# Kernel tuning notes

Measured on AMD Instinct MI355X. Metric: run time of the kernel, lower is better.

Reference implementation:

```python
import jax, jax.numpy as jnp
import numpy as np

NUM_HEADS = 16
THETA = 10000.0


def _rope(x, pos):
    # x: [..., S, D_h], pos: [S] (broadcastable over leading dims)
    dh = x.shape[-1]
    inv_freq = THETA ** (-jnp.arange(0, dh, 2, dtype=x.dtype) / dh)  # [dh/2]
    ang = pos.astype(x.dtype)[..., None] * inv_freq                   # [S, dh/2]
    cos, sin = jnp.cos(ang), jnp.sin(ang)
    x1, x2 = x[..., ::2], x[..., 1::2]
    out = jnp.stack([x1 * cos - x2 * sin, x1 * sin + x2 * cos], axis=-1)
    return out.reshape(x.shape)


def setup_inputs() -> dict:
    key = jax.random.key(0)
    ks = jax.random.split(key, 5)
    B, S, D = 4, 2048, 1024
    return {
        "in_features": jax.random.normal(ks[0], (B, S, D), dtype=jnp.float32),
        "token_positions": jnp.arange(S, dtype=jnp.int32),
        "wq": jax.random.normal(ks[1], (D, D), dtype=jnp.float32) * 0.02,
        "wk": jax.random.normal(ks[2], (D, D), dtype=jnp.float32) * 0.02,
        "wv": jax.random.normal(ks[3], (D, D), dtype=jnp.float32) * 0.02,
        "wo": jax.random.normal(ks[4], (D, D), dtype=jnp.float32) * 0.02,
    }


def reference(in_features, token_positions, wq, wk, wv, wo):
    B, S, D = in_features.shape
    H = NUM_HEADS
    dh = D // H

    def split_heads(y):  # [B,S,D] -> [B,H,S,dh]  ('s (h d) -> h s d')
        return y.reshape(B, S, H, dh).transpose(0, 2, 1, 3)

    Q = split_heads(in_features @ wq.T)
    K = split_heads(in_features @ wk.T)
    V = split_heads(in_features @ wv.T)

    Q = _rope(Q, token_positions)
    K = _rope(K, token_positions)

    scale = 1.0 / jnp.sqrt(jnp.asarray(dh, dtype=Q.dtype))
    scores = jnp.einsum("bhqd,bhkd->bhqk", Q, K) * scale  # [B,H,S,S]
    causal = jnp.tril(jnp.ones((S, S), dtype=bool))
    scores = jnp.where(causal, scores, -jnp.inf)
    attn = jax.nn.softmax(scores, axis=-1)
    out = jnp.einsum("bhqk,bhkd->bhqd", attn, V)          # [B,H,S,dh]
    out = out.transpose(0, 2, 1, 3).reshape(B, S, D)      # 'h s d -> s (h d)'
    return out @ wo.T
```

## Files before the change

### kernel.cpp

```cpp
#include <hip/hip_runtime.h>
#include <hip/hip_bf16.h>
#include <cmath>

#define BB 4
#define SS 2048
#define DD 1024
#define HH 16
#define DH 64
#define LDK 72

typedef __attribute__((ext_vector_type(8))) short short8;
typedef __attribute__((ext_vector_type(4))) float floatx4;
typedef unsigned short u16;
typedef unsigned int u32;

#define QSCALE 0.18033688011112042f

__device__ __forceinline__ u16 f2bf(float f) {
    union { float f; u32 i; } u; u.f = f;
    u32 r = u.i + 0x7fff + ((u.i >> 16) & 1);
    return (u16)(r >> 16);
}

__device__ __forceinline__ u32 pack_bf16(float a, float b) {
    union { float f; u32 i; } ua, ub; ua.f = a; ub.f = b;
    return __builtin_amdgcn_perm(ub.i + 0x8000u, ua.i + 0x8000u, 0x07060302u);
}

#if !__has_builtin(__builtin_amdgcn_exp2f)
#define __builtin_amdgcn_exp2f exp2f
#endif

__global__ __launch_bounds__(256)
void cast_x(const float* __restrict__ s, u16* __restrict__ d)
{
    int i = (blockIdx.x * 256 + threadIdx.x) * 8;
    float4 f0 = *(const float4*)(s + i);
    float4 f1 = *(const float4*)(s + i + 4);
    u32 o[4];
    o[0] = pack_bf16(f0.x, f0.y); o[1] = pack_bf16(f0.z, f0.w);
    o[2] = pack_bf16(f1.x, f1.y); o[3] = pack_bf16(f1.z, f1.w);
    *(short8*)(d + i) = *(short8*)o;
}

__global__ __launch_bounds__(256)
void cast_w(const float* __restrict__ w0, const float* __restrict__ w1,
            const float* __restrict__ w2, const float* __restrict__ w3,
            u16* __restrict__ o0, u16* __restrict__ o1,
            u16* __restrict__ o2, u16* __restrict__ o3)
{
    const float* s = (blockIdx.y == 0) ? w0 : (blockIdx.y == 1) ? w1 : (blockIdx.y == 2) ? w2 : w3;
    u16* d        = (blockIdx.y == 0) ? o0 : (blockIdx.y == 1) ? o1 : (blockIdx.y == 2) ? o2 : o3;
    int i = (blockIdx.x * 256 + threadIdx.x) * 8;
    float4 f0 = *(const float4*)(s + i);
    float4 f1 = *(const float4*)(s + i + 4);
    u32 o[4];
    o[0] = pack_bf16(f0.x, f0.y); o[1] = pack_bf16(f0.z, f0.w);
    o[2] = pack_bf16(f1.x, f1.y); o[3] = pack_bf16(f1.z, f1.w);
    *(short8*)(d + i) = *(short8*)o;
}

__global__ __launch_bounds__(256)
void gemm_qkv(const u16* __restrict__ Xb,
              const u16* __restrict__ Wq, const u16* __restrict__ Wk, const u16* __restrict__ Wv,
              const int* __restrict__ pos,
              u16* __restrict__ Qb, u16* __restrict__ Kb, u16* __restrict__ Vtb)
{
    __shared__ __align__(16) u16 As[128 * LDK];
    __shared__ __align__(16) u16 Bs[128 * LDK];

    const int tid  = threadIdx.x;
    const int lane = tid & 63, w = tid >> 6;
    const int quad = lane >> 4, l16 = lane & 15;
    const int wr = w >> 1, wc = w & 1;
    const int m0 = blockIdx.x * 128, n0 = blockIdx.y * 128;
    const int which = blockIdx.z;
    const u16* __restrict__ W = (which == 0) ? Wq : (which == 1) ? Wk : Wv;

    const int srow = tid >> 3;
    const int skc  = (tid & 7) << 3;

    floatx4 acc[4][4];
    #pragma unroll
    for (int i = 0; i < 4; i++)
        #pragma unroll
        for (int j = 0; j < 4; j++) acc[i][j] = (floatx4)0.f;

    short8 pa[4], pb[4];
    #pragma unroll
    for (int i = 0; i < 4; i++) {
        int row = srow + i * 32;
        pa[i] = *(const short8*)(Xb + (size_t)(m0 + row) * DD + skc);
        pb[i] = *(const short8*)(W  + (size_t)(n0 + row) * DD + skc);
    }

    for (int kb = 0; kb < DD; kb += 64) {
        __syncthreads();
        #pragma unroll
        for (int i = 0; i < 4; i++) {
            int row = srow + i * 32;
            *(short8*)&As[row * LDK + skc] = pa[i];
            *(short8*)&Bs[row * LDK + skc] = pb[i];
        }
        __syncthreads();
        if (kb + 64 < DD) {
            #pragma unroll
            for (int i = 0; i < 4; i++) {
                int row = srow + i * 32;
                pa[i] = *(const short8*)(Xb + (size_t)(m0 + row) * DD + kb + 64 + skc);
                pb[i] = *(const short8*)(W  + (size_t)(n0 + row) * DD + kb + 64 + skc);
            }
        }
        #pragma unroll
        for (int ks = 0; ks < 2; ks++) {
            short8 a[4], b[4];
            #pragma unroll
            for (int mi = 0; mi < 4; mi++)
                a[mi] = *(const short8*)&As[(wr * 64 + mi * 16 + l16) * LDK + ks * 32 + quad * 8];
            #pragma unroll
            for (int ni = 0; ni < 4; ni++)
                b[ni] = *(const short8*)&Bs[(wc * 64 + ni * 16 + l16) * LDK + ks * 32 + quad * 8];
            #pragma unroll
            for (int mi = 0; mi < 4; mi++)
                #pragma unroll
                for (int ni = 0; ni < 4; ni++)
                    acc[mi][ni] = __builtin_amdgcn_mfma_f32_16x16x32_bf16(a[mi], b[ni], acc[mi][ni], 0, 0, 0);
        }
    }

    const int colbase = n0 + wc * 64 + l16;
    const int rowbase = m0 + wr * 64 + quad * 4;
    u16* __restrict__ OutQK = (which == 0) ? Qb : Kb;

    #pragma unroll
    for (int ni = 0; ni < 4; ni++) {
        int col = colbase + ni * 16;
        int h = col >> 6, d = col & 63;
        float fr = __powf(10000.0f, -(float)(d & ~1) / 64.0f);
        bool evn = (d & 1) == 0;
        #pragma unroll
        for (int mi = 0; mi < 4; mi++) {
            int row0 = rowbase + mi * 16;
            if (which == 2) {
                int b = row0 >> 11, s0 = row0 & (SS - 1);
                ushort4 uv;
                uv.x = f2bf(acc[mi][ni][0]);
                uv.y = f2bf(acc[mi][ni][1]);
                uv.z = f2bf(acc[mi][ni][2]);
                uv.w = f2bf(acc[mi][ni][3]);
                *(ushort4*)&Vtb[((size_t)((b * HH + h) * DH + d)) * SS + s0] = uv;
            } else {
                #pragma unroll
                for (int r = 0; r < 4; r++) {
                    int row = row0 + r;
                    int b = row >> 11, s = row & (SS - 1);
                    float v = acc[mi][ni][r];
                    float other = __shfl_xor(v, 1);
                    float ang = (float)pos[s] * fr;
                    float sn, cs;
                    __sincosf(ang, &sn, &cs);
                    float res = evn ? (v * cs - other * sn) : (other * sn + v * cs);
                    if (which == 0) res *= QSCALE;
                    OutQK[((size_t)((b * HH + h) * SS + s)) * DH + d] = f2bf(res);
                }
            }
        }
    }
}

__global__ __launch_bounds__(256)
void flash_mfma(const u16* __restrict__ Qb, const u16* __restrict__ Kb,
                const u16* __restrict__ Vtb, u16* __restrict__ AOb)
{
    __shared__ __align__(16) u16 Ks[64 * LDK];
    __shared__ __align__(16) u16 Vs[64 * LDK];
    __shared__ __align__(16) u16 Ps[4][16 * LDK];

    const int tid  = threadIdx.x;
    const int lane = tid & 63, w = tid >> 6;
    const int quad = lane >> 4, l16 = lane & 15;
    const int qt = blockIdx.x, bh = blockIdx.y;
    const int b = bh >> 4, h = bh & 15;
    const size_t baseQK = (size_t)bh * SS * DH;
    const size_t baseVt = (size_t)bh * DH * SS;

    const int srow = tid >> 3;
    const int skc  = (tid & 7) << 3;

    const u16* Qp = Qb + baseQK + (size_t)(qt * 64 + w * 16 + l16) * DH;
    short8 qf[2];
    qf[0] = *(const short8*)(Qp + quad * 8);
    qf[1] = *(const short8*)(Qp + 32 + quad * 8);

    float m_run = -__builtin_inff(), l_run = 0.f;
    floatx4 oacc[4];
    #pragma unroll
    for (int ni = 0; ni < 4; ni++) oacc[ni] = (floatx4)0.f;

    const int qloc = w * 16 + l16;

    short8 kr[2], vr[2];
    #pragma unroll
    for (int i = 0; i < 2; i++) {
        int row = srow + i * 32;
        kr[i] = *(const short8*)(Kb + baseQK + (size_t)row * DH + skc);
        vr[i] = *(const short8*)(Vtb + baseVt + (size_t)row * SS + skc);
    }

    for (int kt = 0; kt <= qt; kt++) {
        __syncthreads();
        #pragma unroll
        for (int i = 0; i < 2; i++) {
            int row = srow + i * 32;
            *(short8*)&Ks[row * LDK + skc] = kr[i];
            *(short8*)&Vs[row * LDK + skc] = vr[i];
        }
        __syncthreads();
        if (kt < qt) {
            #pragma unroll
            for (int i = 0; i < 2; i++) {
                int row = srow + i * 32;
                kr[i] = *(const short8*)(Kb + baseQK + (size_t)((kt + 1) * 64 + row) * DH + skc);
                vr[i] = *(const short8*)(Vtb + baseVt + (size_t)row * SS + (kt + 1) * 64 + skc);
            }
        }

        floatx4 sacc[4];
        #pragma unroll
        for (int ni = 0; ni < 4; ni++) sacc[ni] = (floatx4)0.f;
        #pragma unroll
        for (int ks = 0; ks < 2; ks++) {
            #pragma unroll
            for (int ni = 0; ni < 4; ni++) {
                short8 kf = *(const short8*)&Ks[(ni * 16 + l16) * LDK + ks * 32 + quad * 8];
                sacc[ni] = __builtin_amdgcn_mfma_f32_16x16x32_bf16(kf, qf[ks], sacc[ni], 0, 0, 0);
            }
        }

        if (kt == qt) {
            #pragma unroll
            for (int ni = 0; ni < 4; ni++)
                #pragma unroll
                for (int r = 0; r < 4; r++)
                    if (ni * 16 + quad * 4 + r > qloc) sacc[ni][r] = -__builtin_inff();
        }

        float mx01 = fmaxf(fmaxf(sacc[0][0], sacc[0][1]), fmaxf(sacc[0][2], sacc[0][3]));
        float mx23 = fmaxf(fmaxf(sacc[1][0], sacc[1][1]), fmaxf(sacc[1][2], sacc[1][3]));
        float mx45 = fmaxf(fmaxf(sacc[2][0], sacc[2][1]), fmaxf(sacc[2][2], sacc[2][3]));
        float mx67 = fmaxf(fmaxf(sacc[3][0], sacc[3][1]), fmaxf(sacc[3][2], sacc[3][3]));
        float mx = fmaxf(fmaxf(mx01, mx23), fmaxf(mx45, mx67));
        mx = fmaxf(mx, __shfl_xor(mx, 16));
        mx = fmaxf(mx, __shfl_xor(mx, 32));
        float mnew = fmaxf(m_run, mx);
        float al = __builtin_amdgcn_exp2f(m_run - mnew);

        float rs = 0.f;
        #pragma unroll
        for (int ni = 0; ni < 4; ni++) {
            float p0 = __builtin_amdgcn_exp2f(sacc[ni][0] - mnew);
            float p1 = __builtin_amdgcn_exp2f(sacc[ni][1] - mnew);
            float p2 = __builtin_amdgcn_exp2f(sacc[ni][2] - mnew);
            float p3 = __builtin_amdgcn_exp2f(sacc[ni][3] - mnew);
            rs += (p0 + p1) + (p2 + p3);
            u32 pk[2];
            pk[0] = pack_bf16(p0, p1);
            pk[1] = pack_bf16(p2, p3);
            *(uint2*)&Ps[w][l16 * LDK + ni * 16 + quad * 4] = *(uint2*)pk;
        }
        l_run = l_run * al + rs;
        m_run = mnew;

        #pragma unroll
        for (int ni = 0; ni < 4; ni++) oacc[ni] *= al;
        #pragma unroll
        for (int ks = 0; ks < 2; ks++) {
            short8 pb = *(const short8*)&Ps[w][l16 * LDK + ks * 32 + quad * 8];
            #pragma unroll
            for (int ni = 0; ni < 4; ni++) {
                short8 vf = *(const short8*)&Vs[(ni * 16 + l16) * LDK + ks * 32 + quad * 8];
                oacc[ni] = __builtin_amdgcn_mfma_f32_16x16x32_bf16(vf, pb, oacc[ni], 0, 0, 0);
            }
        }
    }

    float l_tot = l_run;
    l_tot += __shfl_xor(l_tot, 16);
    l_tot += __shfl_xor(l_tot, 32);
    const float invl = 1.f / l_tot;
    const int srow_o = qt * 64 + w * 16 + l16;
    u16* dst = AOb + (size_t)(b * SS + srow_o) * DD + h * DH;
    #pragma unroll
    for (int ni = 0; ni < 4; ni++) {
        u32 uo[2];
        uo[0] = pack_bf16(oacc[ni][0] * invl, oacc[ni][1] * invl);
        uo[1] = pack_bf16(oacc[ni][2] * invl, oacc[ni][3] * invl);
        *(uint2*)(dst + ni * 16 + quad * 4) = *(uint2*)uo;
    }
}

__global__ __launch_bounds__(256)
void gemm_out(const u16* __restrict__ A, const u16* __restrict__ W, float* __restrict__ C)
{
    __shared__ __align__(16) u16 As[128 * LDK];
    __shared__ __align__(16) u16 Bs[128 * LDK];

    const int tid  = threadIdx.x;
    const int lane = tid & 63, w = tid >> 6;
    const int quad = lane >> 4, l16 = lane & 15;
    const int wr = w >> 1, wc = w & 1;
    const int m0 = blockIdx.x * 128, n0 = blockIdx.y * 128;

    const int srow = tid >> 3;
    const int skc  = (tid & 7) << 3;

    floatx4 acc[4][4];
    #pragma unroll
    for (int i = 0; i < 4; i++)
        #pragma unroll
        for (int j = 0; j < 4; j++) acc[i][j] = (floatx4)0.f;

    short8 pa[4], pb[4];
    #pragma unroll
    for (int i = 0; i < 4; i++) {
        int row = srow + i * 32;
        pa[i] = *(const short8*)(A + (size_t)(m0 + row) * DD + skc);
        pb[i] = *(const short8*)(W + (size_t)(n0 + row) * DD + skc);
    }

    for (int kb = 0; kb < DD; kb += 64) {
        __syncthreads();
        #pragma unroll
        for (int i = 0; i < 4; i++) {
            int row = srow + i * 32;
            *(short8*)&As[row * LDK + skc] = pa[i];
            *(short8*)&Bs[row * LDK + skc] = pb[i];
        }
        __syncthreads();
        if (kb + 64 < DD) {
            #pragma unroll
            for (int i = 0; i < 4; i++) {
                int row = srow + i * 32;
                pa[i] = *(const short8*)(A + (size_t)(m0 + row) * DD + kb + 64 + skc);
                pb[i] = *(const short8*)(W + (size_t)(n0 + row) * DD + kb + 64 + skc);
            }
        }
        #pragma unroll
        for (int ks = 0; ks < 2; ks++) {
            short8 a[4], b[4];
            #pragma unroll
            for (int mi = 0; mi < 4; mi++)
                a[mi] = *(const short8*)&As[(wr * 64 + mi * 16 + l16) * LDK + ks * 32 + quad * 8];
            #pragma unroll
            for (int ni = 0; ni < 4; ni++)
                b[ni] = *(const short8*)&Bs[(wc * 64 + ni * 16 + l16) * LDK + ks * 32 + quad * 8];
            #pragma unroll
            for (int mi = 0; mi < 4; mi++)
                #pragma unroll
                for (int ni = 0; ni < 4; ni++)
                    acc[mi][ni] = __builtin_amdgcn_mfma_f32_16x16x32_bf16(a[mi], b[ni], acc[mi][ni], 0, 0, 0);
        }
    }

    const int colbase = n0 + wc * 64 + l16;
    const int rowbase = m0 + wr * 64 + quad * 4;
    #pragma unroll
    for (int ni = 0; ni < 4; ni++) {
        int col = colbase + ni * 16;
        #pragma unroll
        for (int mi = 0; mi < 4; mi++) {
            int row0 = rowbase + mi * 16;
            #pragma unroll
            for (int r = 0; r < 4; r++)
                C[(size_t)(row0 + r) * DD + col] = acc[mi][ni][r];
        }
    }
}

extern "C" void kernel_launch(void* const* d_in, const int* in_sizes, int n_in,
                              void* d_out, int out_size, void* d_ws, size_t ws_size,
                              hipStream_t stream) {
    const float* X  = (const float*)d_in[0];
    const int* pos  = (const int*)d_in[1];
    const float* wq = (const float*)d_in[2];
    const float* wk = (const float*)d_in[3];
    const float* wv = (const float*)d_in[4];
    const float* wo = (const float*)d_in[5];
    float* out = (float*)d_out;

    const size_t wsz = (size_t)DD * DD;
    const size_t qsz = (size_t)BB * HH * SS * DH;
    u16* Wqb = (u16*)d_ws;
    u16* Wkb = Wqb + wsz;
    u16* Wvb = Wkb + wsz;
    u16* Wob = Wvb + wsz;
    u16* Qb  = Wob + wsz;
    u16* Kb  = Qb + qsz;
    u16* Vtb = Kb + qsz;
    u16* Xb  = Vtb + qsz;
    u16* AOb = Xb;

    dim3 blk(256);
    cast_x<<<dim3(BB * SS * DD / 2048), blk, 0, stream>>>(X, Xb);
    cast_w<<<dim3(DD * DD / 2048, 4), blk, 0, stream>>>(wq, wk, wv, wo, Wqb, Wkb, Wvb, Wob);
    gemm_qkv<<<dim3((BB * SS) / 128, DD / 128, 3), blk, 0, stream>>>(Xb, Wqb, Wkb, Wvb, pos, Qb, Kb, Vtb);
    flash_mfma<<<dim3(SS / 64, BB * HH), blk, 0, stream>>>(Qb, Kb, Vtb, AOb);
    gemm_out<<<dim3((BB * SS) / 128, DD / 128), blk, 0, stream>>>(AOb, Wob, out);
}
```

Measured before the change: 329.8 us.

## Pair mirrored causal query tiles per block to balance flash attention work

Each flash-attention block now handles two query tiles, qt and its mirror (31-qt), so every block does the same amount of causal work. The two tiles share the staged K/V tiles in shared memory, and the grid is halved to 16x64 blocks. This removes the tail imbalance of causal attention and cuts K/V reloads for the lower tile. In exchange it doubles the accumulator registers, which may lower occupancy, and it leaves only 1024 blocks on the device.

```diff
diff --git a/kernel.cpp b/kernel.cpp
--- a/kernel.cpp
+++ b/kernel.cpp
@@ -168,18 +168,84 @@
     }
 }
 
+__device__ __forceinline__ void attn_step(
+    const u16* Ks, const u16* Vs, u16* Psw,
+    const short8* qf, floatx4* oacc, float& m_run, float& l_run,
+    const int l16, const int quad, const bool diag, const int qloc)
+{
+    floatx4 sacc[4];
+    #pragma unroll
+    for (int ni = 0; ni < 4; ni++) sacc[ni] = (floatx4)0.f;
+    #pragma unroll
+    for (int ks = 0; ks < 2; ks++) {
+        #pragma unroll
+        for (int ni = 0; ni < 4; ni++) {
+            short8 kf = *(const short8*)&Ks[(ni * 16 + l16) * LDK + ks * 32 + quad * 8];
+            sacc[ni] = __builtin_amdgcn_mfma_f32_16x16x32_bf16(kf, qf[ks], sacc[ni], 0, 0, 0);
+        }
+    }
+
+    if (diag) {
+        #pragma unroll
+        for (int ni = 0; ni < 4; ni++)
+            #pragma unroll
+            for (int r = 0; r < 4; r++)
+                if (ni * 16 + quad * 4 + r > qloc) sacc[ni][r] = -__builtin_inff();
+    }
+
+    float mx01 = fmaxf(fmaxf(sacc[0][0], sacc[0][1]), fmaxf(sacc[0][2], sacc[0][3]));
+    float mx23 = fmaxf(fmaxf(sacc[1][0], sacc[1][1]), fmaxf(sacc[1][2], sacc[1][3]));
+    float mx45 = fmaxf(fmaxf(sacc[2][0], sacc[2][1]), fmaxf(sacc[2][2], sacc[2][3]));
+    float mx67 = fmaxf(fmaxf(sacc[3][0], sacc[3][1]), fmaxf(sacc[3][2], sacc[3][3]));
+    float mx = fmaxf(fmaxf(mx01, mx23), fmaxf(mx45, mx67));
+    mx = fmaxf(mx, __shfl_xor(mx, 16));
+    mx = fmaxf(mx, __shfl_xor(mx, 32));
+    float mnew = fmaxf(m_run, mx);
+    float al = __builtin_amdgcn_exp2f(m_run - mnew);
+
+    float rs = 0.f;
+    #pragma unroll
+    for (int ni = 0; ni < 4; ni++) {
+        float p0 = __builtin_amdgcn_exp2f(sacc[ni][0] - mnew);
+        float p1 = __builtin_amdgcn_exp2f(sacc[ni][1] - mnew);
+        float p2 = __builtin_amdgcn_exp2f(sacc[ni][2] - mnew);
+        float p3 = __builtin_amdgcn_exp2f(sacc[ni][3] - mnew);
+        rs += (p0 + p1) + (p2 + p3);
+        u32 pk[2];
+        pk[0] = pack_bf16(p0, p1);
+        pk[1] = pack_bf16(p2, p3);
+        *(uint2*)&Psw[l16 * LDK + ni * 16 + quad * 4] = *(uint2*)pk;
+    }
+    l_run = l_run * al + rs;
+    m_run = mnew;
+
+    #pragma unroll
+    for (int ni = 0; ni < 4; ni++) oacc[ni] *= al;
+    #pragma unroll
+    for (int ks = 0; ks < 2; ks++) {
+        short8 pb = *(const short8*)&Psw[l16 * LDK + ks * 32 + quad * 8];
+        #pragma unroll
+        for (int ni = 0; ni < 4; ni++) {
+            short8 vf = *(const short8*)&Vs[(ni * 16 + l16) * LDK + ks * 32 + quad * 8];
+            oacc[ni] = __builtin_amdgcn_mfma_f32_16x16x32_bf16(vf, pb, oacc[ni], 0, 0, 0);
+        }
+    }
+}
+
 __global__ __launch_bounds__(256)
 void flash_mfma(const u16* __restrict__ Qb, const u16* __restrict__ Kb,
                 const u16* __restrict__ Vtb, u16* __restrict__ AOb)
 {
     __shared__ __align__(16) u16 Ks[64 * LDK];
     __shared__ __align__(16) u16 Vs[64 * LDK];
-    __shared__ __align__(16) u16 Ps[4][16 * LDK];
+    __shared__ __align__(16) u16 Ps[4][2][16 * LDK];
 
     const int tid  = threadIdx.x;
     const int lane = tid & 63, w = tid >> 6;
     const int quad = lane >> 4, l16 = lane & 15;
-    const int qt = blockIdx.x, bh = blockIdx.y;
+    const int qtA = blockIdx.x;
+    const int qtB = (SS / 64 - 1) - blockIdx.x;
+    const int bh = blockIdx.y;
     const int b = bh >> 4, h = bh & 15;
     const size_t baseQK = (size_t)bh * SS * DH;
     const size_t baseVt = (size_t)bh * DH * SS;
@@ -187,15 +253,19 @@
     const int srow = tid >> 3;
     const int skc  = (tid & 7) << 3;
 
-    const u16* Qp = Qb + baseQK + (size_t)(qt * 64 + w * 16 + l16) * DH;
-    short8 qf[2];
-    qf[0] = *(const short8*)(Qp + quad * 8);
-    qf[1] = *(const short8*)(Qp + 32 + quad * 8);
-
-    float m_run = -__builtin_inff(), l_run = 0.f;
-    floatx4 oacc[4];
-    #pragma unroll
-    for (int ni = 0; ni < 4; ni++) oacc[ni] = (floatx4)0.f;
+    const u16* QpA = Qb + baseQK + (size_t)(qtA * 64 + w * 16 + l16) * DH;
+    const u16* QpB = Qb + baseQK + (size_t)(qtB * 64 + w * 16 + l16) * DH;
+    short8 qfA[2], qfB[2];
+    qfA[0] = *(const short8*)(QpA + quad * 8);
+    qfA[1] = *(const short8*)(QpA + 32 + quad * 8);
+    qfB[0] = *(const short8*)(QpB + quad * 8);
+    qfB[1] = *(const short8*)(QpB + 32 + quad * 8);
+
+    float mA = -__builtin_inff(), lA = 0.f;
+    float mB = -__builtin_inff(), lB = 0.f;
+    floatx4 oaccA[4], oaccB[4];
+    #pragma unroll
+    for (int ni = 0; ni < 4; ni++) { oaccA[ni] = (floatx4)0.f; oaccB[ni] = (floatx4)0.f; }
 
     const int qloc = w * 16 + l16;
 
@@ -207,7 +277,7 @@
         vr[i] = *(const short8*)(Vtb + baseVt + (size_t)row * SS + skc);
     }
 
-    for (int kt = 0; kt <= qt; kt++) {
+    for (int kt = 0; kt <= qtB; kt++) {
         __syncthreads();
         #pragma unroll
         for (int i = 0; i < 2; i++) {
@@ -216,7 +286,7 @@
             *(short8*)&Vs[row * LDK + skc] = vr[i];
         }
         __syncthreads();
-        if (kt < qt) {
+        if (kt < qtB) {
             #pragma unroll
             for (int i = 0; i < 2; i++) {
                 int row = srow + i * 32;
@@ -225,77 +295,33 @@
             }
         }
 
-        floatx4 sacc[4];
-        #pragma unroll
-        for (int ni = 0; ni < 4; ni++) sacc[ni] = (floatx4)0.f;
-        #pragma unroll
-        for (int ks = 0; ks < 2; ks++) {
-            #pragma unroll
-            for (int ni = 0; ni < 4; ni++) {
-                short8 kf = *(const short8*)&Ks[(ni * 16 + l16) * LDK + ks * 32 + quad * 8];
-                sacc[ni] = __builtin_amdgcn_mfma_f32_16x16x32_bf16(kf, qf[ks], sacc[ni], 0, 0, 0);
-            }
-        }
-
-        if (kt == qt) {
-            #pragma unroll
-            for (int ni = 0; ni < 4; ni++)
-                #pragma unroll
-                for (int r = 0; r < 4; r++)
-                    if (ni * 16 + quad * 4 + r > qloc) sacc[ni][r] = -__builtin_inff();
-        }
-
-        float mx01 = fmaxf(fmaxf(sacc[0][0], sacc[0][1]), fmaxf(sacc[0][2], sacc[0][3]));
-        float mx23 = fmaxf(fmaxf(sacc[1][0], sacc[1][1]), fmaxf(sacc[1][2], sacc[1][3]));
-        float mx45 = fmaxf(fmaxf(sacc[2][0], sacc[2][1]), fmaxf(sacc[2][2], sacc[2][3]));
-        float mx67 = fmaxf(fmaxf(sacc[3][0], sacc[3][1]), fmaxf(sacc[3][2], sacc[3][3]));
-        float mx = fmaxf(fmaxf(mx01, mx23), fmaxf(mx45, mx67));
-        mx = fmaxf(mx, __shfl_xor(mx, 16));
-        mx = fmaxf(mx, __shfl_xor(mx, 32));
-        float mnew = fmaxf(m_run, mx);
-        float al = __builtin_amdgcn_exp2f(m_run - mnew);
-
-        float rs = 0.f;
-        #pragma unroll
-        for (int ni = 0; ni < 4; ni++) {
-            float p0 = __builtin_amdgcn_exp2f(sacc[ni][0] - mnew);
-            float p1 = __builtin_amdgcn_exp2f(sacc[ni][1] - mnew);
-            float p2 = __builtin_amdgcn_exp2f(sacc[ni][2] - mnew);
-            float p3 = __builtin_amdgcn_exp2f(sacc[ni][3] - mnew);
-            rs += (p0 + p1) + (p2 + p3);
-            u32 pk[2];
-            pk[0] = pack_bf16(p0, p1);
-            pk[1] = pack_bf16(p2, p3);
-            *(uint2*)&Ps[w][l16 * LDK + ni * 16 + quad * 4] = *(uint2*)pk;
-        }
-        l_run = l_run * al + rs;
-        m_run = mnew;
-
-        #pragma unroll
-        for (int ni = 0; ni < 4; ni++) oacc[ni] *= al;
-        #pragma unroll
-        for (int ks = 0; ks < 2; ks++) {
-            short8 pb = *(const short8*)&Ps[w][l16 * LDK + ks * 32 + quad * 8];
-            #pragma unroll
-            for (int ni = 0; ni < 4; ni++) {
-                short8 vf = *(const short8*)&Vs[(ni * 16 + l16) * LDK + ks * 32 + quad * 8];
-                oacc[ni] = __builtin_amdgcn_mfma_f32_16x16x32_bf16(vf, pb, oacc[ni], 0, 0, 0);
-            }
-        }
-    }
-
-    float l_tot = l_run;
-    l_tot += __shfl_xor(l_tot, 16);
-    l_tot += __shfl_xor(l_tot, 32);
-    const float invl = 1.f / l_tot;
-    const int srow_o = qt * 64 + w * 16 + l16;
-    u16* dst = AOb + (size_t)(b * SS + srow_o) * DD + h * DH;
+        if (kt <= qtA)
+            attn_step(Ks, Vs, &Ps[w][0][0], qfA, oaccA, mA, lA,
+                      l16, quad, kt == qtA, qloc);
+        attn_step(Ks, Vs, &Ps[w][1][0], qfB, oaccB, mB, lB,
+                  l16, quad, kt == qtB, qloc);
+    }
+
+    float lAt = lA;
+    lAt += __shfl_xor(lAt, 16);
+    lAt += __shfl_xor(lAt, 32);
+    float lBt = lB;
+    lBt += __shfl_xor(lBt, 16);
+    lBt += __shfl_xor(lBt, 32);
+    const float invlA = 1.f / lAt;
+    const float invlB = 1.f / lBt;
+
+    u16* dstA = AOb + (size_t)(b * SS + qtA * 64 + w * 16 + l16) * DD + h * DH;
+    u16* dstB = AOb + (size_t)(b * SS + qtB * 64 + w * 16 + l16) * DD + h * DH;
     #pragma unroll
     for (int ni = 0; ni < 4; ni++) {
         u32 uo[2];
-        uo[0] = pack_bf16(oacc[ni][0] * invl, oacc[ni][1] * invl);
-        uo[1] = pack_bf16(oacc[ni][2] * invl, oacc[ni][3] * invl);
-        *(uint2*)(dst + ni * 16 + quad * 4) = *(uint2*)uo;
+        uo[0] = pack_bf16(oaccA[ni][0] * invlA, oaccA[ni][1] * invlA);
+        uo[1] = pack_bf16(oaccA[ni][2] * invlA, oaccA[ni][3] * invlA);
+        *(uint2*)(dstA + ni * 16 + quad * 4) = *(uint2*)uo;
+        uo[0] = pack_bf16(oaccB[ni][0] * invlB, oaccB[ni][1] * invlB);
+        uo[1] = pack_bf16(oaccB[ni][2] * invlB, oaccB[ni][3] * invlB);
+        *(uint2*)(dstB + ni * 16 + quad * 4) = *(uint2*)uo;
     }
 }
 
@@ -404,6 +430,6 @@
     cast_x<<<dim3(BB * SS * DD / 2048), blk, 0, stream>>>(X, Xb);
     cast_w<<<dim3(DD * DD / 2048, 4), blk, 0, stream>>>(wq, wk, wv, wo, Wqb, Wkb, Wvb, Wob);
     gemm_qkv<<<dim3((BB * SS) / 128, DD / 128, 3), blk, 0, stream>>>(Xb, Wqb, Wkb, Wvb, pos, Qb, Kb, Vtb);
-    flash_mfma<<<dim3(SS / 64, BB * HH), blk, 0, stream>>>(Qb, Kb, Vtb, AOb);
+    flash_mfma<<<dim3(SS / 128, BB * HH), blk, 0, stream>>>(Qb, Kb, Vtb, AOb);
     gemm_out<<<dim3((BB * SS) / 128, DD / 128), blk, 0, stream>>>(AOb, Wob, out);
 }
```

Result: faster. 279.8 us (-15.2%).
